# Kernel tuning notes

Hardware: AMD Instinct MI355X
Metric: run time of the kernel (lower is better)

Reference implementation:

```python
import jax, jax.numpy as jnp
import numpy as np

B, S, DIM, H = 2, 2048, 1024, 16
DK = DIM // H  # 64
NEG = -10000000000.0


def setup_inputs() -> dict:
    key = jax.random.key(0)
    k1, k2, k3, k4, k5, k6 = jax.random.split(key, 6)
    dec_xs = jax.random.normal(k1, (B, S, DIM), dtype=jnp.float32)
    enc_xs = jax.random.normal(k2, (B, S, DIM), dtype=jnp.float32)
    mask = jax.random.randint(k3, (B, S, S), 0, 2, dtype=jnp.int32)
    # torch Linear weights: out = x @ W.T, bias=False
    sc = 1.0 / np.sqrt(DIM)
    Wq = jax.random.normal(k4, (DIM, DIM), dtype=jnp.float32) * sc
    Wkv = jax.random.normal(k5, (2 * DIM, DIM), dtype=jnp.float32) * sc
    Wo = jax.random.normal(k6, (DIM, DIM), dtype=jnp.float32) * sc
    return {"dec_xs": dec_xs, "enc_xs": enc_xs, "Wq": Wq, "Wkv": Wkv, "Wo": Wo, "mask": mask}


def reference(dec_xs, enc_xs, Wq, Wkv, Wo, mask):
    b, s, dim = enc_xs.shape
    qs = dec_xs @ Wq.T                      # [b,s,dim]  (dropout inactive in eval)
    kv = enc_xs @ Wkv.T                     # [b,s,2*dim]
    ks, vs = jnp.split(kv, 2, axis=-1)
    # head layout: view(b, s, dk, h) -- heads LAST, as in the original
    qs = qs.reshape(b, s, DK, H)
    ks = ks.reshape(b, s, DK, H)
    vs = vs.reshape(b, s, DK, H)
    scores = jnp.einsum('bqdh,bkdh->bqkh', qs, ks) / np.sqrt(DK)
    scores = jnp.where(mask[..., None] == 0, NEG, scores)
    weights = jax.nn.softmax(scores, axis=-2)  # softmax over key axis
    out = jnp.einsum('bqkh,bkdh->bqdh', weights, vs).reshape(b, s, dim)
    return out @ Wo.T
```

## Files before the change

kernel.cpp:

```cpp
#include <hip/hip_runtime.h>
#include <hip/hip_bf16.h>

#define BB 2
#define SS 2048
#define DIMM 1024
#define HH 16
#define DKK 64
#define QSCALE 0.18033688011112042592f

using bf16 = __hip_bfloat16;
typedef __attribute__((ext_vector_type(8))) short v8s;
typedef __attribute__((ext_vector_type(4))) short v4s;
typedef __attribute__((ext_vector_type(4))) float f32x4;

__device__ __forceinline__ void cvt4(const float* __restrict__ s,
                                     bf16* __restrict__ d, int idx) {
  const float4 f = ((const float4*)s)[idx];
  bf16 t[4] = {__float2bfloat16(f.x), __float2bfloat16(f.y),
               __float2bfloat16(f.z), __float2bfloat16(f.w)};
  *(v4s*)(d + (size_t)idx * 4) = *(const v4s*)t;
}

__global__ __launch_bounds__(256) void convert_pack_kernel(
    const float* __restrict__ dec, const float* __restrict__ enc,
    const float* __restrict__ Wq, const float* __restrict__ Wkv,
    const float* __restrict__ Wo, const int* __restrict__ mask,
    bf16* __restrict__ decb, bf16* __restrict__ encb, bf16* __restrict__ Wqb,
    bf16* __restrict__ Wkvb, bf16* __restrict__ Wob,
    unsigned long long* __restrict__ mp) {
  const int gid = blockIdx.x * 256 + threadIdx.x;
  const int NT = 256 * 1024;
#pragma unroll
  for (int i = 0; i < 4; ++i) cvt4(dec, decb, gid + i * NT);
#pragma unroll
  for (int i = 0; i < 4; ++i) cvt4(enc, encb, gid + i * NT);
  cvt4(Wq, Wqb, gid);
#pragma unroll
  for (int i = 0; i < 2; ++i) cvt4(Wkv, Wkvb, gid + i * NT);
  cvt4(Wo, Wob, gid);
  const int lane = threadIdx.x & 63;
  const int wave_id = gid >> 6;
  for (int i = 0; i < 32; ++i) {
    const size_t w = (size_t)wave_id * 32 + i;
    const unsigned long long bm = __ballot(mask[w * 64 + lane] != 0);
    if (lane == 0) mp[w] = bm;
  }
}

__global__ __launch_bounds__(256) void proj_gemm_kernel(
    const bf16* __restrict__ decb, const bf16* __restrict__ encb,
    const bf16* __restrict__ Wqb, const bf16* __restrict__ Wkvb,
    bf16* __restrict__ Qr, bf16* __restrict__ Kr, bf16* __restrict__ Vt) {
  __shared__ __align__(16) bf16 As[128][72];
  __shared__ __align__(16) bf16 Bs[128][72];
  const int t = threadIdx.x;
  const int wave = t >> 6, lane = t & 63;
  const int quad = lane >> 4, l15 = lane & 15;
  const int wm = (wave >> 1) * 64, wn = (wave & 1) * 64;
  const int bx = blockIdx.x;
  const int kind = bx >> 3;
  const int g = bx & 7;
  const int m0 = blockIdx.y * 128;

  const bf16* Asrc = (kind == 0) ? decb : encb;
  const bf16* Wsrc = (kind == 0) ? Wqb : Wkvb;

  const int sr = t >> 2;
  const int sc = (t & 3) * 16;
  const int wr0 = sr * 16 + g * 2 + ((kind == 2) ? DIMM : 0);
  const int wr1 = sr * 16 + g * 2 + 1 + ((kind == 2) ? DIMM : 0);

  v8s apf[4], bpf[4];
  auto loadA = [&](int kc) {
    const bf16* p0 = Asrc + (size_t)(m0 + sr) * DIMM + kc + sc;
    apf[0] = ((const v8s*)p0)[0];
    apf[1] = ((const v8s*)p0)[1];
    const bf16* p1 = Asrc + (size_t)(m0 + sr + 64) * DIMM + kc + sc;
    apf[2] = ((const v8s*)p1)[0];
    apf[3] = ((const v8s*)p1)[1];
  };
  auto loadB = [&](int kc) {
    const bf16* q0 = Wsrc + (size_t)wr0 * DIMM + kc + sc;
    bpf[0] = ((const v8s*)q0)[0];
    bpf[1] = ((const v8s*)q0)[1];
    const bf16* q1 = Wsrc + (size_t)wr1 * DIMM + kc + sc;
    bpf[2] = ((const v8s*)q1)[0];
    bpf[3] = ((const v8s*)q1)[1];
  };

  f32x4 acc[4][4] = {};
  loadA(0);
  loadB(0);

  for (int kc = 0; kc < DIMM; kc += 64) {
    __syncthreads();
    *(v8s*)&As[sr][sc] = apf[0];
    *(v8s*)&As[sr][sc + 8] = apf[1];
    *(v8s*)&As[sr + 64][sc] = apf[2];
    *(v8s*)&As[sr + 64][sc + 8] = apf[3];
    *(v8s*)&Bs[sr][sc] = bpf[0];
    *(v8s*)&Bs[sr][sc + 8] = bpf[1];
    *(v8s*)&Bs[sr + 64][sc] = bpf[2];
    *(v8s*)&Bs[sr + 64][sc + 8] = bpf[3];
    if (kc + 64 < DIMM) {
      loadA(kc + 64);
      loadB(kc + 64);
    }
    __syncthreads();
#pragma unroll
    for (int ks = 0; ks < 2; ++ks) {
      v8s af[4], bfr[4];
#pragma unroll
      for (int i = 0; i < 4; ++i)
        af[i] = *(const v8s*)&As[wm + i * 16 + l15][ks * 32 + quad * 8];
#pragma unroll
      for (int j = 0; j < 4; ++j)
        bfr[j] = *(const v8s*)&Bs[wn + j * 16 + l15][ks * 32 + quad * 8];
#pragma unroll
      for (int i = 0; i < 4; ++i)
#pragma unroll
        for (int j = 0; j < 4; ++j)
          acc[i][j] = __builtin_amdgcn_mfma_f32_16x16x32_bf16(
              af[i], bfr[j], acc[i][j], 0, 0, 0);
    }
  }

#pragma unroll
  for (int i = 0; i < 4; ++i) {
#pragma unroll
    for (int r = 0; r < 4; ++r) {
      const int m = m0 + wm + i * 16 + quad * 4 + r;
#pragma unroll
      for (int j = 0; j < 4; ++j) {
        const int c = wn + j * 16 + l15;
        const int np = g * 128 + c;
        const float v = acc[i][j][r];
        if (kind == 0) {
          Qr[(size_t)m * DIMM + np] = __float2bfloat16(v * QSCALE);
        } else if (kind == 1) {
          Kr[(size_t)m * DIMM + np] = __float2bfloat16(v);
        } else {
          const int h = np >> 6, d = np & 63;
          const int b = m >> 11, s = m & (SS - 1);
          Vt[(((size_t)b * HH + h) * DKK + d) * SS + s] = __float2bfloat16(v);
        }
      }
    }
  }
}

__global__ __launch_bounds__(256) void out_gemm_kernel(
    const bf16* __restrict__ A, const bf16* __restrict__ W,
    float* __restrict__ out) {
  __shared__ __align__(16) bf16 As[128][72];
  __shared__ __align__(16) bf16 Bs[64][72];
  const int t = threadIdx.x;
  const int wave = t >> 6, lane = t & 63;
  const int quad = lane >> 4, l15 = lane & 15;
  const int wm = (wave >> 1) * 64, wn = (wave & 1) * 32;
  const int n0 = blockIdx.x * 64;
  const int m0 = blockIdx.y * 128;
  const int sr = t >> 2;
  const int sc = (t & 3) * 16;

  v8s ar[4], br[2];
  auto loadA = [&](int kc) {
#pragma unroll
    for (int rr = 0; rr < 2; ++rr) {
      const bf16* p = A + (size_t)(m0 + sr + rr * 64) * DIMM + kc + sc;
#pragma unroll
      for (int i = 0; i < 2; ++i) ar[rr * 2 + i] = ((const v8s*)p)[i];
    }
  };
  auto loadB = [&](int kc) {
    const bf16* p = W + (size_t)(n0 + sr) * DIMM + kc + sc;
#pragma unroll
    for (int i = 0; i < 2; ++i) br[i] = ((const v8s*)p)[i];
  };

  f32x4 acc[4][2] = {};
  loadA(0);
  loadB(0);
  for (int kc = 0; kc < DIMM; kc += 64) {
    __syncthreads();
#pragma unroll
    for (int rr = 0; rr < 2; ++rr) {
      *(v8s*)&As[sr + rr * 64][sc] = ar[rr * 2 + 0];
      *(v8s*)&As[sr + rr * 64][sc + 8] = ar[rr * 2 + 1];
    }
    *(v8s*)&Bs[sr][sc] = br[0];
    *(v8s*)&Bs[sr][sc + 8] = br[1];
    if (kc + 64 < DIMM) {
      loadA(kc + 64);
      loadB(kc + 64);
    }
    __syncthreads();
#pragma unroll
    for (int ks = 0; ks < 2; ++ks) {
      v8s af[4], bfr[2];
#pragma unroll
      for (int i = 0; i < 4; ++i)
        af[i] = *(const v8s*)&As[wm + i * 16 + l15][ks * 32 + quad * 8];
#pragma unroll
      for (int j = 0; j < 2; ++j)
        bfr[j] = *(const v8s*)&Bs[wn + j * 16 + l15][ks * 32 + quad * 8];
#pragma unroll
      for (int i = 0; i < 4; ++i)
#pragma unroll
        for (int j = 0; j < 2; ++j)
          acc[i][j] = __builtin_amdgcn_mfma_f32_16x16x32_bf16(
              af[i], bfr[j], acc[i][j], 0, 0, 0);
    }
  }

#pragma unroll
  for (int i = 0; i < 4; ++i) {
#pragma unroll
    for (int r = 0; r < 4; ++r) {
      const int m = m0 + wm + i * 16 + quad * 4 + r;
#pragma unroll
      for (int j = 0; j < 2; ++j) {
        const int n = n0 + wn + j * 16 + l15;
        out[(size_t)m * DIMM + n] = acc[i][j][r];
      }
    }
  }
}

__global__ __launch_bounds__(512) void attn_kernel(
    const bf16* __restrict__ Qr, const bf16* __restrict__ Kr,
    const bf16* __restrict__ Vt, const unsigned long long* __restrict__ mp,
    bf16* __restrict__ Ar) {
  __shared__ __align__(16) bf16 Ks[2][64][72];
  __shared__ __align__(16) bf16 Vs[2][64][72];
  __shared__ __align__(16) bf16 Ps[8][16][72];

  const int t = threadIdx.x;
  const int wave = t >> 6, lane = t & 63;
  const int quad = lane >> 4, l15 = lane & 15;

  const int bx = blockIdx.x;
  const int xcd = bx & 7, j = bx >> 3;
  const int g = (xcd << 2) | (j & 3);
  const int tile = j >> 2;
  const int h = g & 15, b = g >> 4;

  const int qw = tile * 128 + wave * 16;
  const size_t bhv = ((size_t)b * HH + h) * DKK;

  const bf16* qrow = Qr + ((size_t)(b * SS + qw + l15)) * DIMM + h * 64;
  const v8s aq0 = *(const v8s*)(qrow + quad * 8);
  const v8s aq1 = *(const v8s*)(qrow + 32 + quad * 8);

  f32x4 o[4] = {};
  float lsum[4] = {0.f, 0.f, 0.f, 0.f};

  const int id0 = t * 8;
  const int r0 = id0 >> 6, c0 = id0 & 63;

  auto loadK = [&](int kt) {
    return *(const v8s*)(Kr + ((size_t)(b * SS + kt * 64 + r0)) * DIMM +
                         h * 64 + c0);
  };
  auto loadV = [&](int kt) {
    return *(const v8s*)(Vt + (bhv + r0) * SS + kt * 64 + c0);
  };

  v8s kreg = loadK(0), vreg = loadV(0);
  *(v8s*)&Ks[0][r0][c0] = kreg;
  *(v8s*)&Vs[0][r0][c0] = vreg;
  kreg = loadK(1);
  vreg = loadV(1);

  int p = 0;
  for (int kt = 0; kt < 32; ++kt) {
    __syncthreads();
    if (kt < 31) {
      *(v8s*)&Ks[p ^ 1][r0][c0] = kreg;
      *(v8s*)&Vs[p ^ 1][r0][c0] = vreg;
      if (kt < 30) {
        kreg = loadK(kt + 2);
        vreg = loadV(kt + 2);
      }
    }

    unsigned long long mw[4];
#pragma unroll
    for (int r = 0; r < 4; ++r)
      mw[r] = mp[((size_t)b * SS + qw + quad * 4 + r) * 32 + kt] >> l15;

    f32x4 sc[4];
#pragma unroll
    for (int n = 0; n < 4; ++n) {
      const v8s bk0 = *(const v8s*)&Ks[p][n * 16 + l15][quad * 8];
      const v8s bk1 = *(const v8s*)&Ks[p][n * 16 + l15][32 + quad * 8];
      f32x4 z = {0.f, 0.f, 0.f, 0.f};
      z = __builtin_amdgcn_mfma_f32_16x16x32_bf16(aq0, bk0, z, 0, 0, 0);
      sc[n] = __builtin_amdgcn_mfma_f32_16x16x32_bf16(aq1, bk1, z, 0, 0, 0);
    }

#pragma unroll
    for (int n = 0; n < 4; ++n)
#pragma unroll
      for (int r = 0; r < 4; ++r) {
        const bool keep = (mw[r] >> (n * 16)) & 1ULL;
        const float pw = keep ? __builtin_amdgcn_exp2f(sc[n][r]) : 0.f;
        sc[n][r] = pw;
        lsum[r] += pw;
      }

#pragma unroll
    for (int n = 0; n < 4; ++n)
#pragma unroll
      for (int r = 0; r < 4; ++r)
        Ps[wave][quad * 4 + r][n * 16 + l15] = __float2bfloat16(sc[n][r]);
    const v8s ap0 = *(const v8s*)&Ps[wave][l15][quad * 8];
    const v8s ap1 = *(const v8s*)&Ps[wave][l15][32 + quad * 8];

#pragma unroll
    for (int n = 0; n < 4; ++n) {
      const v8s bv0 = *(const v8s*)&Vs[p][n * 16 + l15][quad * 8];
      const v8s bv1 = *(const v8s*)&Vs[p][n * 16 + l15][32 + quad * 8];
      o[n] = __builtin_amdgcn_mfma_f32_16x16x32_bf16(ap0, bv0, o[n], 0, 0, 0);
      o[n] = __builtin_amdgcn_mfma_f32_16x16x32_bf16(ap1, bv1, o[n], 0, 0, 0);
    }
    p ^= 1;
  }

#pragma unroll
  for (int r = 0; r < 4; ++r) {
    float l = lsum[r];
    l += __shfl_xor(l, 1);
    l += __shfl_xor(l, 2);
    l += __shfl_xor(l, 4);
    l += __shfl_xor(l, 8);
    const float inv = 1.f / l;
    const size_t row = (size_t)b * SS + qw + quad * 4 + r;
#pragma unroll
    for (int n = 0; n < 4; ++n) {
      const int d = n * 16 + l15;
      Ar[row * DIMM + d * 16 + h] = __float2bfloat16(o[n][r] * inv);
    }
  }
}

extern "C" void kernel_launch(void* const* d_in, const int* in_sizes, int n_in,
                              void* d_out, int out_size, void* d_ws,
                              size_t ws_size, hipStream_t stream) {
  const float* dec = (const float*)d_in[0];
  const float* enc = (const float*)d_in[1];
  const float* Wq = (const float*)d_in[2];
  const float* Wkv = (const float*)d_in[3];
  const float* Wo = (const float*)d_in[4];
  const int* mask = (const int*)d_in[5];
  float* out = (float*)d_out;

  bf16* decb = (bf16*)d_out;
  bf16* Wqb = (bf16*)((char*)d_out + ((size_t)2 * SS * DIMM * 2));

  char* ws = (char*)d_ws;
  size_t off = 0;
  bf16* encb = (bf16*)(ws + off);
  bf16* Ar = (bf16*)(ws + off);   off += (size_t)2 * SS * DIMM * 2;
  bf16* Wkvb = (bf16*)(ws + off); off += (size_t)2 * DIMM * DIMM * 2;
  bf16* Wob = (bf16*)(ws + off);  off += (size_t)DIMM * DIMM * 2;
  bf16* Qr = (bf16*)(ws + off);   off += (size_t)2 * SS * DIMM * 2;
  bf16* Kr = (bf16*)(ws + off);   off += (size_t)2 * SS * DIMM * 2;
  bf16* Vt = (bf16*)(ws + off);   off += (size_t)2 * SS * DIMM * 2;
  unsigned long long* mp = (unsigned long long*)(ws + off);

  dim3 blk(256);
  convert_pack_kernel<<<dim3(1024), blk, 0, stream>>>(
      dec, enc, Wq, Wkv, Wo, mask, decb, encb, Wqb, Wkvb, Wob, mp);
  proj_gemm_kernel<<<dim3(24, 32), blk, 0, stream>>>(decb, encb, Wqb, Wkvb, Qr,
                                                     Kr, Vt);
  attn_kernel<<<dim3(512), dim3(512), 0, stream>>>(Qr, Kr, Vt, mp, Ar);
  out_gemm_kernel<<<dim3(16, 32), blk, 0, stream>>>(Ar, Wob, out);
}
```

Baseline: 274.3 us.

## Permute Wo columns to head-major and swap GEMM operands for V transpose

```diff
diff --git a/kernel.cpp b/kernel.cpp
--- a/kernel.cpp
+++ b/kernel.cpp
@@ -37,7 +37,17 @@
   cvt4(Wq, Wqb, gid);
 #pragma unroll
   for (int i = 0; i < 2; ++i) cvt4(Wkv, Wkvb, gid + i * NT);
-  cvt4(Wo, Wob, gid);
+  {
+    const int n = gid >> 8;
+    const int c4 = (gid & 255) * 4;
+    const int h = c4 >> 6, d0 = c4 & 63;
+    const float* src = Wo + (size_t)n * DIMM + h;
+    bf16 t[4];
+#pragma unroll
+    for (int i2 = 0; i2 < 4; ++i2)
+      t[i2] = __float2bfloat16(src[(d0 + i2) * 16]);
+    *(v4s*)(Wob + (size_t)n * DIMM + c4) = *(const v4s*)t;
+  }
   const int lane = threadIdx.x & 63;
   const int wave_id = gid >> 6;
   for (int i = 0; i < 32; ++i) {
@@ -62,35 +72,47 @@
   const int g = bx & 7;
   const int m0 = blockIdx.y * 128;
 
-  const bf16* Asrc = (kind == 0) ? decb : encb;
-  const bf16* Wsrc = (kind == 0) ? Wqb : Wkvb;
-
   const int sr = t >> 2;
   const int sc = (t & 3) * 16;
-  const int wr0 = sr * 16 + g * 2 + ((kind == 2) ? DIMM : 0);
-  const int wr1 = sr * 16 + g * 2 + 1 + ((kind == 2) ? DIMM : 0);
+  const int voff = (kind == 2) ? DIMM : 0;
+  const int wr0 = sr * 16 + g * 2 + voff;
+  const int wr1 = sr * 16 + g * 2 + 1 + voff;
+
+  const bf16* arow0;
+  const bf16* arow1;
+  const bf16* brow0;
+  const bf16* brow1;
+  if (kind == 0) {
+    arow0 = decb + (size_t)(m0 + sr) * DIMM;
+    arow1 = decb + (size_t)(m0 + sr + 64) * DIMM;
+    brow0 = Wqb + (size_t)wr0 * DIMM;
+    brow1 = Wqb + (size_t)wr1 * DIMM;
+  } else if (kind == 1) {
+    arow0 = encb + (size_t)(m0 + sr) * DIMM;
+    arow1 = encb + (size_t)(m0 + sr + 64) * DIMM;
+    brow0 = Wkvb + (size_t)wr0 * DIMM;
+    brow1 = Wkvb + (size_t)wr1 * DIMM;
+  } else {
+    arow0 = Wkvb + (size_t)wr0 * DIMM;
+    arow1 = Wkvb + (size_t)wr1 * DIMM;
+    brow0 = encb + (size_t)(m0 + sr) * DIMM;
+    brow1 = encb + (size_t)(m0 + sr + 64) * DIMM;
+  }
 
   v8s apf[4], bpf[4];
-  auto loadA = [&](int kc) {
-    const bf16* p0 = Asrc + (size_t)(m0 + sr) * DIMM + kc + sc;
-    apf[0] = ((const v8s*)p0)[0];
-    apf[1] = ((const v8s*)p0)[1];
-    const bf16* p1 = Asrc + (size_t)(m0 + sr + 64) * DIMM + kc + sc;
-    apf[2] = ((const v8s*)p1)[0];
-    apf[3] = ((const v8s*)p1)[1];
-  };
-  auto loadB = [&](int kc) {
-    const bf16* q0 = Wsrc + (size_t)wr0 * DIMM + kc + sc;
-    bpf[0] = ((const v8s*)q0)[0];
-    bpf[1] = ((const v8s*)q0)[1];
-    const bf16* q1 = Wsrc + (size_t)wr1 * DIMM + kc + sc;
-    bpf[2] = ((const v8s*)q1)[0];
-    bpf[3] = ((const v8s*)q1)[1];
+  auto loadAB = [&](int kc) {
+    apf[0] = ((const v8s*)(arow0 + kc + sc))[0];
+    apf[1] = ((const v8s*)(arow0 + kc + sc))[1];
+    apf[2] = ((const v8s*)(arow1 + kc + sc))[0];
+    apf[3] = ((const v8s*)(arow1 + kc + sc))[1];
+    bpf[0] = ((const v8s*)(brow0 + kc + sc))[0];
+    bpf[1] = ((const v8s*)(brow0 + kc + sc))[1];
+    bpf[2] = ((const v8s*)(brow1 + kc + sc))[0];
+    bpf[3] = ((const v8s*)(brow1 + kc + sc))[1];
   };
 
   f32x4 acc[4][4] = {};
-  loadA(0);
-  loadB(0);
+  loadAB(0);
 
   for (int kc = 0; kc < DIMM; kc += 64) {
     __syncthreads();
@@ -102,10 +124,7 @@
     *(v8s*)&Bs[sr][sc + 8] = bpf[1];
     *(v8s*)&Bs[sr + 64][sc] = bpf[2];
     *(v8s*)&Bs[sr + 64][sc + 8] = bpf[3];
-    if (kc + 64 < DIMM) {
-      loadA(kc + 64);
-      loadB(kc + 64);
-    }
+    if (kc + 64 < DIMM) loadAB(kc + 64);
     __syncthreads();
 #pragma unroll
     for (int ks = 0; ks < 2; ++ks) {
@@ -129,19 +148,20 @@
   for (int i = 0; i < 4; ++i) {
 #pragma unroll
     for (int r = 0; r < 4; ++r) {
-      const int m = m0 + wm + i * 16 + quad * 4 + r;
+      const int mm = wm + i * 16 + quad * 4 + r;
 #pragma unroll
       for (int j = 0; j < 4; ++j) {
-        const int c = wn + j * 16 + l15;
-        const int np = g * 128 + c;
+        const int nn = wn + j * 16 + l15;
         const float v = acc[i][j][r];
         if (kind == 0) {
-          Qr[(size_t)m * DIMM + np] = __float2bfloat16(v * QSCALE);
+          Qr[(size_t)(m0 + mm) * DIMM + g * 128 + nn] =
+              __float2bfloat16(v * QSCALE);
         } else if (kind == 1) {
-          Kr[(size_t)m * DIMM + np] = __float2bfloat16(v);
+          Kr[(size_t)(m0 + mm) * DIMM + g * 128 + nn] = __float2bfloat16(v);
         } else {
-          const int h = np >> 6, d = np & 63;
-          const int b = m >> 11, s = m & (SS - 1);
+          const int h = g * 2 + (mm >> 6), d = mm & 63;
+          const int sn = m0 + nn;
+          const int b = sn >> 11, s = sn & (SS - 1);
           Vt[(((size_t)b * HH + h) * DKK + d) * SS + s] = __float2bfloat16(v);
         }
       }
@@ -338,8 +358,7 @@
     const size_t row = (size_t)b * SS + qw + quad * 4 + r;
 #pragma unroll
     for (int n = 0; n < 4; ++n) {
-      const int d = n * 16 + l15;
-      Ar[row * DIMM + d * 16 + h] = __float2bfloat16(o[n][r] * inv);
+      Ar[row * DIMM + h * 64 + n * 16 + l15] = __float2bfloat16(o[n][r] * inv);
     }
   }
 }
```

After: 255.5 us. -6.8%, faster.
